# Performance work log

Hardware: AMD Instinct MI355X
Metric: run time of the kernel (lower is better)

The kernel has to match this reference:

```python
import jax, jax.numpy as jnp
import numpy as np

SIGMA = 2.0  # gaussian kernel std, matches init kwarg
N, H, W = 200, 448, 448
NUM_CLASSES = 80


def setup_inputs() -> dict:
    key = jax.random.key(0)
    k1, k2, k3 = jax.random.split(key, 3)
    seg_masks = (jax.random.uniform(k1, (N, H, W)) < 0.3).astype(jnp.float32)
    # scores in descending order (matrix_nms assumes sorted input)
    cate_scores = jnp.sort(jax.random.uniform(k2, (N,), dtype=jnp.float32))[::-1]
    cate_labels = jax.random.randint(k3, (N,), 0, NUM_CLASSES)
    return {"seg_masks": seg_masks, "cate_scores": cate_scores, "cate_labels": cate_labels}


def reference(seg_masks, cate_scores, cate_labels):
    n = seg_masks.shape[0]
    flat = seg_masks.reshape(n, -1).astype(jnp.float32)          # (n, HW)
    sum_masks = flat.sum(axis=1)                                  # (n,)
    inter = flat @ flat.T                                         # (n, n) mask intersection
    union = sum_masks[None, :] + sum_masks[:, None] - inter
    iou = jnp.triu(inter / union, k=1)                            # upper-tri IoU
    same_label = jnp.triu(
        (cate_labels[None, :] == cate_labels[:, None]).astype(jnp.float32), k=1
    )
    decay_iou = iou * same_label                                  # (n, n)
    # compensate IoU: per-candidate max overlap with a higher-scoring same-class mask
    compensate_iou = decay_iou.max(axis=0)                        # (n,)
    # gaussian decay: exp(-sigma*iou^2) / exp(-sigma*comp_i^2), min over rows
    decay_matrix = jnp.exp(SIGMA * (compensate_iou[:, None] ** 2 - decay_iou ** 2))
    decay_coefficient = decay_matrix.min(axis=0)                  # (n,)
    return cate_scores * decay_coefficient
```

## Files before the change

### kernel.cpp

```cpp
#include <hip/hip_runtime.h>
#include <cstdint>
#include <cstddef>

#define N_INST 200
#define HWPIX (448 * 448)
#define W64 3136
#define SIGMA 2.0f
#define NCHUNK 8
#define NTILE 325

#define P_SLAB  (N_INST * N_INST)
#define OFF_P   5017600
#define OFF_SP  (OFF_P + NCHUNK * P_SLAB * 4)
#define OFF_CMP (OFF_SP + NCHUNK * 256 * 4)

__global__ void __launch_bounds__(64)
pack_kernel(const float* __restrict__ seg, uint64_t* __restrict__ packed) {
    const int t = threadIdx.x;
    const float4* s4 = (const float4*)(seg + (size_t)blockIdx.y * HWPIX
                                           + (size_t)blockIdx.x * 4096);
    float4 v[16];
#pragma unroll
    for (int s = 0; s < 16; ++s) v[s] = s4[s * 64 + t];
    uint64_t m = 0;
#pragma unroll
    for (int s = 0; s < 16; ++s) {
        uint32_t b = 0;
        b |= (v[s].x > 0.5f) ? 1u : 0u;
        b |= (v[s].y > 0.5f) ? 2u : 0u;
        b |= (v[s].z > 0.5f) ? 4u : 0u;
        b |= (v[s].w > 0.5f) ? 8u : 0u;
        m |= (uint64_t)b << (4 * s);
    }
    packed[(size_t)blockIdx.y * W64 + blockIdx.x * 64 + t] = m;
}

__global__ void pair_kernel(const uint64_t* __restrict__ packed,
                            int* __restrict__ P,
                            int* __restrict__ SP) {
    const int wt   = blockIdx.x * 4 + (threadIdx.x >> 6);
    const int lane = threadIdx.x & 63;
    const int t     = wt >> 3;
    const int chunk = wt & 7;

    int jt = (int)((sqrtf((float)(8 * t + 1)) - 1.0f) * 0.5f);
    while ((jt + 1) * (jt + 2) / 2 <= t) ++jt;
    while (jt * (jt + 1) / 2 > t) --jt;
    const int it = t - jt * (jt + 1) / 2;
    const int i0 = 8 * it, j0 = 8 * jt;

    const int ks = (chunk * 49) >> 3;
    const int ke = ((chunk + 1) * 49) >> 3;

    const uint64_t* A = packed + (size_t)i0 * W64;
    const uint64_t* B = packed + (size_t)j0 * W64;

    int c[64];
#pragma unroll
    for (int x = 0; x < 64; ++x) c[x] = 0;

    for (int kb = ks; kb < ke; ++kb) {
        const int k = kb * 64 + lane;
        uint64_t a[8], b[8];
#pragma unroll
        for (int r = 0; r < 8; ++r) { a[r] = A[k + r * W64]; b[r] = B[k + r * W64]; }
#pragma unroll
        for (int r = 0; r < 8; ++r)
#pragma unroll
            for (int cc = 0; cc < 8; ++cc)
                c[r * 8 + cc] += __popcll(a[r] & b[cc]);
    }

    int p[32];
#pragma unroll
    for (int m = 0; m < 32; ++m) p[m] = c[2 * m] + (c[2 * m + 1] << 16);
#pragma unroll
    for (int off = 1; off < 64; off <<= 1) {
#pragma unroll
        for (int m = 0; m < 32; ++m) p[m] += __shfl_xor(p[m], off, 64);
    }

    if (lane == 0) {
#pragma unroll
        for (int r = 0; r < 8; ++r) {
#pragma unroll
            for (int cc = 0; cc < 8; ++cc) {
                const int idx = r * 8 + cc;
                const int val = (idx & 1) ? (int)(((unsigned)p[idx >> 1]) >> 16)
                                          : (p[idx >> 1] & 0xFFFF);
                const int i = i0 + r, j = j0 + cc;
                if (i < j)       P[chunk * P_SLAB + j * N_INST + i] = val;
                else if (i == j) SP[chunk * 256 + i] = val;
            }
        }
    }
}

#define OFF_DT  (OFF_CMP + 1024)

__global__ void iou_comp_kernel(const int* __restrict__ P,
                                const int* __restrict__ SP,
                                const int* __restrict__ labels,
                                float* __restrict__ DTf,
                                float* __restrict__ comp) {
    const int j = blockIdx.x;
    const int t = threadIdx.x;
    int sj = 0;
#pragma unroll
    for (int cch = 0; cch < NCHUNK; ++cch) sj += SP[cch * 256 + j];
    const int lj = labels[j];
    float m = 0.0f;
    for (int i = t; i < j; i += 64) {
        int inter = 0;
#pragma unroll
        for (int cch = 0; cch < NCHUNK; ++cch)
            inter += P[cch * P_SLAB + j * N_INST + i];
        int si = 0;
#pragma unroll
        for (int cch = 0; cch < NCHUNK; ++cch) si += SP[cch * 256 + i];
        const float iou = (float)inter / (float)(si + sj - inter);
        const float d = (labels[i] == lj) ? iou : 0.0f;
        DTf[j * N_INST + i] = d;
        m = fmaxf(m, d);
    }
#pragma unroll
    for (int off = 1; off < 64; off <<= 1) m = fmaxf(m, __shfl_xor(m, off, 64));
    if (t == 0) comp[j] = m;
}

__global__ void finalize_kernel(const float* __restrict__ DTf,
                                const float* __restrict__ comp,
                                const float* __restrict__ scores,
                                float* __restrict__ out) {
    const int j = blockIdx.x;
    const int t = threadIdx.x;
    const float* row = DTf + (size_t)j * N_INST;
    float mn = 3.4e38f;
    for (int i = t; i < N_INST; i += 64) {
        const float ci = comp[i];
        float v = ci * ci;
        if (i < j) { const float d = row[i]; v -= d * d; }
        mn = fminf(mn, v);
    }
#pragma unroll
    for (int off = 1; off < 64; off <<= 1) mn = fminf(mn, __shfl_xor(mn, off, 64));
    if (t == 0) out[j] = scores[j] * expf(SIGMA * mn);
}

extern "C" void kernel_launch(void* const* d_in, const int* in_sizes, int n_in,
                              void* d_out, int out_size, void* d_ws, size_t ws_size,
                              hipStream_t stream) {
    const float* seg    = (const float*)d_in[0];
    const float* scores = (const float*)d_in[1];
    const int*   labels = (const int*)d_in[2];
    float* out = (float*)d_out;

    uint64_t* packed = (uint64_t*)d_ws;
    int*      P      = (int*)((char*)d_ws + OFF_P);
    int*      SP     = (int*)((char*)d_ws + OFF_SP);
    float*    comp   = (float*)((char*)d_ws + OFF_CMP);
    float*    DTf    = (float*)((char*)d_ws + OFF_DT);

    {
        dim3 grid(49, N_INST);
        pack_kernel<<<grid, 64, 0, stream>>>(seg, packed);
    }
    pair_kernel<<<NTILE * NCHUNK / 4, 256, 0, stream>>>(packed, P, SP);
    iou_comp_kernel<<<N_INST, 64, 0, stream>>>(P, SP, labels, DTf, comp);
    finalize_kernel<<<N_INST, 64, 0, stream>>>(DTf, comp, scores, out);
}
```

Measured before the change: 250.1 us.

## Fuse IoU and decay epilogue into one block; use nontemporal integer mask loads

The two epilogue kernels are merged into a single 1024-thread block. The compensate max is kept in shared memory and the IoU is recomputed from the pair counts, so the DTf matrix is no longer written and read back and one launch is removed. The pack kernel now reads the masks as raw uint32 with nontemporal loads and tests for nonzero bits instead of doing a float compare. That test relies on masks being exactly 0.0 or 1.0, and -0.0 would count as set. Running the epilogue on one block serialises that work onto a single CU.

After: 270.5 us. 8.2% more time.

```diff
diff --git a/kernel.cpp b/kernel.cpp
--- a/kernel.cpp
+++ b/kernel.cpp
@@ -12,24 +12,26 @@
 #define P_SLAB  (N_INST * N_INST)
 #define OFF_P   5017600
 #define OFF_SP  (OFF_P + NCHUNK * P_SLAB * 4)
-#define OFF_CMP (OFF_SP + NCHUNK * 256 * 4)
+
+typedef unsigned int uint4v __attribute__((ext_vector_type(4)));
 
 __global__ void __launch_bounds__(64)
-pack_kernel(const float* __restrict__ seg, uint64_t* __restrict__ packed) {
+pack_kernel(const uint32_t* __restrict__ seg, uint64_t* __restrict__ packed) {
     const int t = threadIdx.x;
-    const float4* s4 = (const float4*)(seg + (size_t)blockIdx.y * HWPIX
+    const uint4v* s4 = (const uint4v*)(seg + (size_t)blockIdx.y * HWPIX
                                            + (size_t)blockIdx.x * 4096);
-    float4 v[16];
+    uint4v v[16];
 #pragma unroll
-    for (int s = 0; s < 16; ++s) v[s] = s4[s * 64 + t];
+    for (int s = 0; s < 16; ++s)
+        v[s] = __builtin_nontemporal_load(&s4[s * 64 + t]);
     uint64_t m = 0;
 #pragma unroll
     for (int s = 0; s < 16; ++s) {
         uint32_t b = 0;
-        b |= (v[s].x > 0.5f) ? 1u : 0u;
-        b |= (v[s].y > 0.5f) ? 2u : 0u;
-        b |= (v[s].z > 0.5f) ? 4u : 0u;
-        b |= (v[s].w > 0.5f) ? 8u : 0u;
+        b |= v[s].x ? 1u : 0u;
+        b |= v[s].y ? 2u : 0u;
+        b |= v[s].z ? 4u : 0u;
+        b |= v[s].w ? 8u : 0u;
         m |= (uint64_t)b << (4 * s);
     }
     packed[(size_t)blockIdx.y * W64 + blockIdx.x * 64 + t] = m;
@@ -96,61 +98,76 @@
     }
 }
 
-#define OFF_DT  (OFF_CMP + 1024)
+__global__ void __launch_bounds__(1024)
+epilogue_kernel(const int* __restrict__ P,
+                const int* __restrict__ SP,
+                const int* __restrict__ labels,
+                const float* __restrict__ scores,
+                float* __restrict__ out) {
+    __shared__ float ssum[N_INST];
+    __shared__ int   lab[N_INST];
+    __shared__ float comp[N_INST];
+    const int tid  = threadIdx.x;
+    const int wv   = tid >> 6;
+    const int lane = tid & 63;
 
-__global__ void iou_comp_kernel(const int* __restrict__ P,
-                                const int* __restrict__ SP,
-                                const int* __restrict__ labels,
-                                float* __restrict__ DTf,
-                                float* __restrict__ comp) {
-    const int j = blockIdx.x;
-    const int t = threadIdx.x;
-    int sj = 0;
+    if (tid < N_INST) {
+        int s = 0;
 #pragma unroll
-    for (int cch = 0; cch < NCHUNK; ++cch) sj += SP[cch * 256 + j];
-    const int lj = labels[j];
-    float m = 0.0f;
-    for (int i = t; i < j; i += 64) {
-        int inter = 0;
+        for (int cch = 0; cch < NCHUNK; ++cch) s += SP[cch * 256 + tid];
+        ssum[tid] = (float)s;
+        lab[tid]  = labels[tid];
+    }
+    __syncthreads();
+
+    for (int j = wv; j < N_INST; j += 16) {
+        const float sj = ssum[j];
+        const int   lj = lab[j];
+        float m = 0.0f;
+        for (int i = lane; i < j; i += 64) {
+            int inter = 0;
 #pragma unroll
-        for (int cch = 0; cch < NCHUNK; ++cch)
-            inter += P[cch * P_SLAB + j * N_INST + i];
-        int si = 0;
+            for (int cch = 0; cch < NCHUNK; ++cch)
+                inter += P[cch * P_SLAB + j * N_INST + i];
+            const float iou = (float)inter / (ssum[i] + sj - (float)inter);
+            m = fmaxf(m, (lab[i] == lj) ? iou : 0.0f);
+        }
 #pragma unroll
-        for (int cch = 0; cch < NCHUNK; ++cch) si += SP[cch * 256 + i];
-        const float iou = (float)inter / (float)(si + sj - inter);
-        const float d = (labels[i] == lj) ? iou : 0.0f;
-        DTf[j * N_INST + i] = d;
-        m = fmaxf(m, d);
+        for (int off = 1; off < 64; off <<= 1)
+            m = fmaxf(m, __shfl_xor(m, off, 64));
+        if (lane == 0) comp[j] = m;
     }
+    __syncthreads();
+
+    for (int j = wv; j < N_INST; j += 16) {
+        const float sj = ssum[j];
+        const int   lj = lab[j];
+        float mn = 3.4e38f;
+        for (int i = lane; i < N_INST; i += 64) {
+            const float ci = comp[i];
+            float v = ci * ci;
+            if (i < j) {
+                int inter = 0;
 #pragma unroll
-    for (int off = 1; off < 64; off <<= 1) m = fmaxf(m, __shfl_xor(m, off, 64));
-    if (t == 0) comp[j] = m;
-}
-
-__global__ void finalize_kernel(const float* __restrict__ DTf,
-                                const float* __restrict__ comp,
-                                const float* __restrict__ scores,
-                                float* __restrict__ out) {
-    const int j = blockIdx.x;
-    const int t = threadIdx.x;
-    const float* row = DTf + (size_t)j * N_INST;
-    float mn = 3.4e38f;
-    for (int i = t; i < N_INST; i += 64) {
-        const float ci = comp[i];
-        float v = ci * ci;
-        if (i < j) { const float d = row[i]; v -= d * d; }
-        mn = fminf(mn, v);
+                for (int cch = 0; cch < NCHUNK; ++cch)
+                    inter += P[cch * P_SLAB + j * N_INST + i];
+                const float iou = (float)inter / (ssum[i] + sj - (float)inter);
+                const float d = (lab[i] == lj) ? iou : 0.0f;
+                v -= d * d;
+            }
+            mn = fminf(mn, v);
+        }
+#pragma unroll
+        for (int off = 1; off < 64; off <<= 1)
+            mn = fminf(mn, __shfl_xor(mn, off, 64));
+        if (lane == 0) out[j] = scores[j] * expf(SIGMA * mn);
     }
-#pragma unroll
-    for (int off = 1; off < 64; off <<= 1) mn = fminf(mn, __shfl_xor(mn, off, 64));
-    if (t == 0) out[j] = scores[j] * expf(SIGMA * mn);
 }
 
 extern "C" void kernel_launch(void* const* d_in, const int* in_sizes, int n_in,
                               void* d_out, int out_size, void* d_ws, size_t ws_size,
                               hipStream_t stream) {
-    const float* seg    = (const float*)d_in[0];
+    const uint32_t* seg = (const uint32_t*)d_in[0];
     const float* scores = (const float*)d_in[1];
     const int*   labels = (const int*)d_in[2];
     float* out = (float*)d_out;
@@ -158,14 +175,11 @@
     uint64_t* packed = (uint64_t*)d_ws;
     int*      P      = (int*)((char*)d_ws + OFF_P);
     int*      SP     = (int*)((char*)d_ws + OFF_SP);
-    float*    comp   = (float*)((char*)d_ws + OFF_CMP);
-    float*    DTf    = (float*)((char*)d_ws + OFF_DT);
 
     {
         dim3 grid(49, N_INST);
         pack_kernel<<<grid, 64, 0, stream>>>(seg, packed);
     }
     pair_kernel<<<NTILE * NCHUNK / 4, 256, 0, stream>>>(packed, P, SP);
-    iou_comp_kernel<<<N_INST, 64, 0, stream>>>(P, SP, labels, DTf, comp);
-    finalize_kernel<<<N_INST, 64, 0, stream>>>(DTf, comp, scores, out);
+    epilogue_kernel<<<1, 1024, 0, stream>>>(P, SP, labels, scores, out);
 }
```
